# Performance work log

Hardware: AMD Instinct MI355X
Metric: run time of the kernel (lower is better)

## Reference

```python
import jax, jax.numpy as jnp
import numpy as np

N = 100000   # skill_num
D = 128      # skill_embed_dim
E = 500000   # edges per relation
S = 16384    # queried skills
NEG_SLOPE = 0.2


def _gat(x, edge_index, W, att_src, att_dst, bias):
    # PyG GATConv, heads=1, add_self_loops=True, eval mode (no dropout)
    n = x.shape[0]
    loops = jnp.arange(n)
    src = jnp.concatenate([edge_index[0], loops])
    dst = jnp.concatenate([edge_index[1], loops])
    h = x @ W                              # [N, D]
    a_src = h @ att_src                    # [N]
    a_dst = h @ att_dst                    # [N]
    e = jax.nn.leaky_relu(a_src[src] + a_dst[dst], NEG_SLOPE)  # [E+N]
    emax = jax.ops.segment_max(e, dst, num_segments=n)
    ex = jnp.exp(e - emax[dst])
    denom = jax.ops.segment_sum(ex, dst, num_segments=n)
    alpha = ex / (denom[dst] + 1e-16)
    out = jax.ops.segment_sum(alpha[:, None] * h[src], dst, num_segments=n)
    return out + bias


def _sage(x, edge_index, Wl, bl, Wr):
    # PyG SAGEConv, aggr='mean', root_weight=True (lin_r has no bias)
    n = x.shape[0]
    src, dst = edge_index[0], edge_index[1]
    ones = jnp.ones((src.shape[0],), dtype=x.dtype)
    deg = jax.ops.segment_sum(ones, dst, num_segments=n)
    agg = jax.ops.segment_sum(x[src], dst, num_segments=n)
    agg = agg / jnp.maximum(deg, 1.0)[:, None]
    return agg @ Wl + bl + x @ Wr


def setup_inputs() -> dict:
    key = jax.random.key(0)
    ks = jax.random.split(key, 16)
    sc = 1.0 / np.sqrt(D)
    inp = {
        "s": jax.random.randint(ks[0], (S,), 0, N),
        "t_s": 0,
        "t_e": 12,
        "ei_parent": jax.random.randint(ks[1], (2, E), 0, N),
        "ei_child": jax.random.randint(ks[2], (2, E), 0, N),
        "ei_relate": jax.random.randint(ks[3], (2, E), 0, N),
        "emb": jax.random.normal(ks[4], (N, D), dtype=jnp.float32),
        # GAT is_parent params
        "Wp": jax.random.normal(ks[5], (D, D), dtype=jnp.float32) * sc,
        "asp": jax.random.normal(ks[6], (D,), dtype=jnp.float32) * sc,
        "adp": jax.random.normal(ks[7], (D,), dtype=jnp.float32) * sc,
        "bp": jnp.zeros((D,), dtype=jnp.float32),
        # GAT is_child params
        "Wc": jax.random.normal(ks[8], (D, D), dtype=jnp.float32) * sc,
        "asc": jax.random.normal(ks[9], (D,), dtype=jnp.float32) * sc,
        "adc": jax.random.normal(ks[10], (D,), dtype=jnp.float32) * sc,
        "bc": jnp.zeros((D,), dtype=jnp.float32),
        # SAGE relate params
        "Wl": jax.random.normal(ks[11], (D, D), dtype=jnp.float32) * sc,
        "bl": jnp.zeros((D,), dtype=jnp.float32),
        "Wr": jax.random.normal(ks[12], (D, D), dtype=jnp.float32) * sc,
    }
    return inp


def reference(s, t_s, t_e, ei_parent, ei_child, ei_relate, emb,
              Wp, asp, adp, bp, Wc, asc, adc, bc, Wl, bl, Wr):
    out_parent = _gat(emb, ei_parent, Wp, asp, adp, bp)
    out_child = _gat(emb, ei_child, Wc, asc, adc, bc)
    out_relate = _sage(emb, ei_relate, Wl, bl, Wr)
    # HeteroConv(aggr='mean') over the three relation outputs
    node_out = (out_parent + out_child + out_relate) / 3.0
    return node_out[s, :]
```

## Files before the change

### kernel.cpp

```cpp
#include <hip/hip_runtime.h>

#define D 128
#define CAP 64
#define OVF_CAP 1024

typedef short bf16x8 __attribute__((ext_vector_type(8)));
typedef short short4v __attribute__((ext_vector_type(4)));
typedef float f32x4 __attribute__((ext_vector_type(4)));

__device__ __forceinline__ short f2bf(float f) {
  unsigned u = __builtin_bit_cast(unsigned, f);
  unsigned r = (u + 0x7fffu + ((u >> 16) & 1u)) >> 16;
  return (short)r;
}
__device__ __forceinline__ float bflo(unsigned r) {
  return __builtin_bit_cast(float, r << 16);
}
__device__ __forceinline__ float bfhi(unsigned r) {
  return __builtin_bit_cast(float, r & 0xffff0000u);
}


__global__ void k_setup(const float* __restrict__ Wp, const float* __restrict__ asp,
                        const float* __restrict__ adp, const float* __restrict__ Wc,
                        const float* __restrict__ asc, const float* __restrict__ adc,
                        const float* __restrict__ bp, const float* __restrict__ bc,
                        const float* __restrict__ bl, const float* __restrict__ Wl,
                        const float* __restrict__ Wr,
                        float* __restrict__ v, short* __restrict__ wpack,
                        int* __restrict__ qid, int* __restrict__ counters,
                        int* __restrict__ deg3, int N, int S3) {
  int i = blockIdx.x * blockDim.x + threadIdx.x;
  int stride = gridDim.x * blockDim.x;
  for (int k = i; k < N; k += stride) qid[k] = -1;
  for (int k = i; k < S3; k += stride) deg3[k] = 0;
  if (i < 16) counters[i] = 0;

  for (int idx = i; idx < 16 * 8 * 64 * 8; idx += stride) {
    int j    = idx & 7;
    int lane = (idx >> 3) & 63;
    int nt   = (idx >> 9) & 7;
    int kt   = idx >> 12;
    int o = kt >> 2;
    int c = (kt & 3) * 32 + (lane >> 4) * 8 + j;
    int n = nt * 16 + (lane & 15);
    const float* W = (o == 0) ? Wp : (o == 1) ? Wc : (o == 2) ? Wl : Wr;
    wpack[idx] = f2bf(W[c * D + n]);
  }

  if (blockIdx.x == 0 && threadIdx.x < 128) {
    int k = threadIdx.x;
    float s0 = 0.f, s1 = 0.f, s2 = 0.f, s3 = 0.f;
    for (int d = 0; d < D; ++d) {
      float wp = Wp[k * D + d], wc = Wc[k * D + d];
      s0 += wp * asp[d]; s1 += wp * adp[d];
      s2 += wc * asc[d]; s3 += wc * adc[d];
    }
    v[k] = s0; v[D + k] = s1; v[2 * D + k] = s2; v[3 * D + k] = s3;
    v[4 * D + k] = bp[k] + bc[k] + bl[k];
  }
}

__global__ void k_pre(const int* __restrict__ s, int* __restrict__ qid,
                      int* __restrict__ uniq, int* __restrict__ counters, int S,
                      const float* __restrict__ emb, const float* __restrict__ v,
                      float* __restrict__ a_sp, float* __restrict__ a_dp,
                      float* __restrict__ a_sc, float* __restrict__ a_dc,
                      unsigned* __restrict__ ebf, int N) {
  int gtid = blockIdx.x * blockDim.x + threadIdx.x;
  if (gtid < S) {
    int n = s[gtid];
    if (atomicCAS(&qid[n], -1, -2) == -1) {
      int u = atomicAdd(&counters[0], 1);
      uniq[u] = n;
      qid[n] = u;
    }
  }
  int node = gtid >> 6;
  int lane = threadIdx.x & 63;
  if (node >= N) return;
  float2 x2 = ((const float2*)(emb + (size_t)node * D))[lane];
  unsigned p = ((unsigned)(unsigned short)f2bf(x2.x)) |
               (((unsigned)(unsigned short)f2bf(x2.y)) << 16);
  ebf[(size_t)node * 64 + lane] = p;
  float2 v0 = ((const float2*)(v))[lane];
  float2 v1 = ((const float2*)(v + D))[lane];
  float2 v2 = ((const float2*)(v + 2 * D))[lane];
  float2 v3 = ((const float2*)(v + 3 * D))[lane];
  float s0 = x2.x * v0.x + x2.y * v0.y;
  float s1 = x2.x * v1.x + x2.y * v1.y;
  float s2 = x2.x * v2.x + x2.y * v2.y;
  float s3 = x2.x * v3.x + x2.y * v3.y;
  for (int o = 32; o > 0; o >>= 1) {
    s0 += __shfl_down(s0, o);
    s1 += __shfl_down(s1, o);
    s2 += __shfl_down(s2, o);
    s3 += __shfl_down(s3, o);
  }
  if (lane == 0) { a_sp[node] = s0; a_dp[node] = s1; a_sc[node] = s2; a_dc[node] = s3; }
}

__global__ void __launch_bounds__(256) k_filter(
    const int* __restrict__ eiP, const int* __restrict__ eiC, const int* __restrict__ eiR,
    const int* __restrict__ qid,
    int* __restrict__ bktP, int* __restrict__ bktC, int* __restrict__ bktR,
    int* __restrict__ degP, int* __restrict__ degC, int* __restrict__ degR,
    int2* __restrict__ ovf, int* __restrict__ counters, int E) {
  int rel = blockIdx.y;
  const int* ei = (rel == 0) ? eiP : (rel == 1) ? eiC : eiR;
  int* bkt      = (rel == 0) ? bktP : (rel == 1) ? bktC : bktR;
  int* deg      = (rel == 0) ? degP : (rel == 1) ? degC : degR;
  int e = blockIdx.x * 256 + threadIdx.x;
  if (e >= E) return;
  int dst = ei[E + e];
  int u = qid[dst];
  if (u < 0) return;
  int src = ei[e];
  int pos = atomicAdd(&deg[u], 1);
  if (pos < CAP) {
    bkt[u * CAP + pos] = src;
  } else {
    int o = atomicAdd(&counters[4 + rel], 1);
    if (o < OVF_CAP) { int2 t; t.x = src; t.y = u; ovf[rel * OVF_CAP + o] = t; }
  }
}

__global__ void __launch_bounds__(256) k_accum(
    const int* __restrict__ bktP, const int* __restrict__ bktC, const int* __restrict__ bktR,
    const int* __restrict__ degP, const int* __restrict__ degC, const int* __restrict__ degR,
    const float* __restrict__ a_sp, const float* __restrict__ a_dp,
    const float* __restrict__ a_sc, const float* __restrict__ a_dc,
    const unsigned* __restrict__ ebf, const int* __restrict__ uniq,
    const int* __restrict__ counters, const int2* __restrict__ ovf,
    float* __restrict__ num_p, float* __restrict__ num_c, float* __restrict__ sum_r,
    float* __restrict__ den_p, float* __restrict__ den_c) {
  int U = counters[0];
  int u = blockIdx.x * 4 + (threadIdx.x >> 6);
  if (u >= U) return;
  int lane = threadIdx.x & 63;
  int rel = blockIdx.y;
  const int* bkt = (rel == 0) ? bktP : (rel == 1) ? bktC : bktR;
  const int* deg = (rel == 0) ? degP : (rel == 1) ? degC : degR;
  float* num     = (rel == 0) ? num_p : (rel == 1) ? num_c : sum_r;

  int m = deg[u];
  int mc = (m < CAP) ? m : CAP;
  int L = counters[4 + rel];
  if (L > OVF_CAP) L = OVF_CAP;
  const int* b0 = bkt + u * CAP;
  float2 acc; acc.x = 0.f; acc.y = 0.f;

  int srcl = (lane < mc) ? b0[lane] : 0;
  float wl = 0.f;
  bool gat = (rel != 2);
  float denl = 0.f;
  if (gat) {
    const float* a_s = (rel == 0) ? a_sp : a_sc;
    const float* a_d = (rel == 0) ? a_dp : a_dc;
    int n = uniq[u];
    float adn = a_d[n];
    if (lane < mc) {
      float t = a_s[srcl] + adn;
      t = t >= 0.f ? t : 0.2f * t;
      wl = __expf(t);
    }
    denl = wl;
  } else {
    wl = (lane < mc) ? 1.f : 0.f;
  }

  int i = 0;
  for (; i + 4 <= mc; i += 4) {
    int s0 = __shfl(srcl, i),     s1 = __shfl(srcl, i + 1);
    int s2 = __shfl(srcl, i + 2), s3 = __shfl(srcl, i + 3);
    float w0 = __shfl(wl, i),     w1 = __shfl(wl, i + 1);
    float w2 = __shfl(wl, i + 2), w3 = __shfl(wl, i + 3);
    unsigned r0 = ebf[(size_t)s0 * 64 + lane];
    unsigned r1 = ebf[(size_t)s1 * 64 + lane];
    unsigned r2 = ebf[(size_t)s2 * 64 + lane];
    unsigned r3 = ebf[(size_t)s3 * 64 + lane];
    acc.x += w0 * bflo(r0) + w1 * bflo(r1) + w2 * bflo(r2) + w3 * bflo(r3);
    acc.y += w0 * bfhi(r0) + w1 * bfhi(r1) + w2 * bfhi(r2) + w3 * bfhi(r3);
  }
  for (; i < mc; ++i) {
    int si = __shfl(srcl, i);
    float wi = __shfl(wl, i);
    unsigned r = ebf[(size_t)si * 64 + lane];
    acc.x += wi * bflo(r);
    acc.y += wi * bfhi(r);
  }

  if (gat) {
    const float* a_s = (rel == 0) ? a_sp : a_sc;
    const float* a_d = (rel == 0) ? a_dp : a_dc;
    float adn = a_d[uniq[u]];
    float denx = 0.f;
    for (int l = 0; l < L; ++l) {
      int2 ov = ovf[rel * OVF_CAP + l];
      if (ov.y == u) {
        float t = a_s[ov.x] + adn;
        t = t >= 0.f ? t : 0.2f * t;
        float w = __expf(t);
        unsigned r = ebf[(size_t)ov.x * 64 + lane];
        acc.x += w * bflo(r); acc.y += w * bfhi(r);
        if (lane == 0) denx += w;
      }
    }
    for (int o = 32; o > 0; o >>= 1) denl += __shfl_down(denl, o);
    if (lane == 0) { ((rel == 0) ? den_p : den_c)[u] = denl + denx; }
  } else {
    for (int l = 0; l < L; ++l) {
      int2 ov = ovf[2 * OVF_CAP + l];
      if (ov.y == u) {
        unsigned r = ebf[(size_t)ov.x * 64 + lane];
        acc.x += bflo(r); acc.y += bfhi(r);
      }
    }
  }
  ((float2*)(num + (size_t)u * D))[lane] = acc;
}

__global__ void __launch_bounds__(256) k_final(
    const float* __restrict__ num_p, const float* __restrict__ num_c,
    const float* __restrict__ sum_r, const float* __restrict__ emb,
    const int* __restrict__ uniq, const int* __restrict__ counters,
    const float* __restrict__ a_sp, const float* __restrict__ a_dp,
    const float* __restrict__ a_sc, const float* __restrict__ a_dc,
    const float* __restrict__ den_p, const float* __restrict__ den_c,
    const int* __restrict__ deg_r, const float* __restrict__ vvec,
    const short* __restrict__ wpack, float* __restrict__ outU) {
  __shared__ short A_lds[16 * 64 * 8];
  int U = counters[0];
  int u0 = blockIdx.x * 16;
  if (u0 >= U) return;
  int tid = threadIdx.x;

  {
    int m = tid >> 4;
    int oc = tid & 15;
    int u = u0 + m;
    int uu = (u < U) ? u : u0;
    int n = uniq[uu];
    float tP = a_sp[n] + a_dp[n]; tP = tP >= 0.f ? tP : 0.2f * tP;
    float wP = __expf(tP);
    float rP = 1.f / (den_p[uu] + wP);
    float tC = a_sc[n] + a_dc[n]; tC = tC >= 0.f ? tC : 0.2f * tC;
    float wC = __expf(tC);
    float rC = 1.f / (den_c[uu] + wC);
    float dg = (float)deg_r[uu]; if (dg < 1.f) dg = 1.f;
    float rdeg = 1.f / dg;
#pragma unroll
    for (int half = 0; half < 2; ++half) {
      int c4 = oc * 8 + half * 4;
      int q = (c4 >> 3) & 3;
      int j0 = c4 & 7;
      int ktc = c4 >> 5;
      float4 e4  = *(const float4*)(emb   + (size_t)n  * D + c4);
      float4 np4 = *(const float4*)(num_p + (size_t)uu * D + c4);
      float4 nc4 = *(const float4*)(num_c + (size_t)uu * D + c4);
      float4 sr4 = *(const float4*)(sum_r + (size_t)uu * D + c4);
      float4 z[4];
      z[0].x = (np4.x + wP * e4.x) * rP; z[0].y = (np4.y + wP * e4.y) * rP;
      z[0].z = (np4.z + wP * e4.z) * rP; z[0].w = (np4.w + wP * e4.w) * rP;
      z[1].x = (nc4.x + wC * e4.x) * rC; z[1].y = (nc4.y + wC * e4.y) * rC;
      z[1].z = (nc4.z + wC * e4.z) * rC; z[1].w = (nc4.w + wC * e4.w) * rC;
      z[2].x = sr4.x * rdeg; z[2].y = sr4.y * rdeg;
      z[2].z = sr4.z * rdeg; z[2].w = sr4.w * rdeg;
      z[3] = e4;
#pragma unroll
      for (int o = 0; o < 4; ++o) {
        int kt = o * 4 + ktc;
        short4v s4;
        s4.x = f2bf(z[o].x); s4.y = f2bf(z[o].y);
        s4.z = f2bf(z[o].z); s4.w = f2bf(z[o].w);
        *(short4v*)&A_lds[(kt * 64 + q * 16 + m) * 8 + j0] = s4;
      }
    }
  }
  __syncthreads();

  int w = tid >> 6;
  int lane = tid & 63;
  f32x4 acc0 = {0.f, 0.f, 0.f, 0.f};
  f32x4 acc1 = {0.f, 0.f, 0.f, 0.f};
  const bf16x8* wp = (const bf16x8*)wpack;
#pragma unroll
  for (int kt = 0; kt < 16; ++kt) {
    bf16x8 a  = *(const bf16x8*)&A_lds[(kt * 64 + lane) * 8];
    bf16x8 b0 = wp[(kt * 8 + 2 * w) * 64 + lane];
    bf16x8 b1 = wp[(kt * 8 + 2 * w + 1) * 64 + lane];
    acc0 = __builtin_amdgcn_mfma_f32_16x16x32_bf16(a, b0, acc0, 0, 0, 0);
    acc1 = __builtin_amdgcn_mfma_f32_16x16x32_bf16(a, b1, acc1, 0, 0, 0);
  }

  int col0 = 2 * w * 16 + (lane & 15);
  int col1 = col0 + 16;
  int r0 = (lane >> 4) * 4;
  float b0v = vvec[4 * D + col0] * (1.f / 3.f);
  float b1v = vvec[4 * D + col1] * (1.f / 3.f);
#pragma unroll
  for (int reg = 0; reg < 4; ++reg) {
    int u = u0 + r0 + reg;
    if (u < U) {
      outU[(size_t)u * D + col0] = acc0[reg] * (1.f / 3.f) + b0v;
      outU[(size_t)u * D + col1] = acc1[reg] * (1.f / 3.f) + b1v;
    }
  }
}

__global__ void k_gather(const int* __restrict__ s, const int* __restrict__ qid,
                         const float* __restrict__ outU, float* __restrict__ out, int S) {
  int idx = blockIdx.x * blockDim.x + threadIdx.x;
  if (idx >= S * D) return;
  int i = idx >> 7;
  int d = idx & (D - 1);
  int u = qid[s[i]];
  out[idx] = outU[(size_t)u * D + d];
}


extern "C" void kernel_launch(void* const* d_in, const int* in_sizes, int n_in,
                              void* d_out, int out_size, void* d_ws, size_t ws_size,
                              hipStream_t stream) {
  const int*   s   = (const int*)d_in[0];
  const int*   eip = (const int*)d_in[3];
  const int*   eic = (const int*)d_in[4];
  const int*   eir = (const int*)d_in[5];
  const float* emb = (const float*)d_in[6];
  const float* Wp  = (const float*)d_in[7];
  const float* asp = (const float*)d_in[8];
  const float* adp = (const float*)d_in[9];
  const float* bp  = (const float*)d_in[10];
  const float* Wc  = (const float*)d_in[11];
  const float* asc = (const float*)d_in[12];
  const float* adc = (const float*)d_in[13];
  const float* bc  = (const float*)d_in[14];
  const float* Wl  = (const float*)d_in[15];
  const float* bl  = (const float*)d_in[16];
  const float* Wr  = (const float*)d_in[17];
  float* out = (float*)d_out;

  const int S = in_sizes[0];
  const int E = in_sizes[3] / 2;
  const int N = in_sizes[6] / D;

  char* base = (char*)d_ws;
  size_t off = 0;
  auto carve = [&](size_t bytes) -> char* {
    char* q = base + off;
    off += (bytes + 255) & ~(size_t)255;
    return q;
  };
  float*    a_sp     = (float*)carve((size_t)N * 4);
  float*    a_dp     = (float*)carve((size_t)N * 4);
  float*    a_sc     = (float*)carve((size_t)N * 4);
  float*    a_dc     = (float*)carve((size_t)N * 4);
  int*      qid      = (int*)carve((size_t)N * 4);
  unsigned* ebf      = (unsigned*)carve((size_t)N * 64 * 4);
  int*      uniq     = (int*)carve((size_t)S * 4);
  int*      counters = (int*)carve(64);
  float*    vvec     = (float*)carve(5 * D * 4);
  short*    wpack    = (short*)carve((size_t)16 * 8 * 64 * 8 * 2);
  float*    num_p    = (float*)carve((size_t)S * D * 4);
  float*    den_p    = (float*)carve((size_t)S * 4);
  float*    num_c    = (float*)carve((size_t)S * D * 4);
  float*    den_c    = (float*)carve((size_t)S * 4);
  float*    sum_r    = (float*)carve((size_t)S * D * 4);
  float*    outU     = (float*)carve((size_t)S * D * 4);
  int*      degP     = (int*)carve((size_t)S * 4);
  int*      degC     = (int*)carve((size_t)S * 4);
  int*      degR     = (int*)carve((size_t)S * 4);
  int*      bktP     = (int*)carve((size_t)S * CAP * 4);
  int*      bktC     = (int*)carve((size_t)S * CAP * 4);
  int*      bktR     = (int*)carve((size_t)S * CAP * 4);
  int2*     ovf      = (int2*)carve((size_t)3 * OVF_CAP * 8);
  (void)ws_size; (void)n_in; (void)out_size;

  k_setup<<<256, 256, 0, stream>>>(Wp, asp, adp, Wc, asc, adc, bp, bc, bl, Wl, Wr,
                                   vvec, wpack, qid, counters, degP, N, 3 * S);

  k_pre<<<(N * 64 + 255) / 256, 256, 0, stream>>>(s, qid, uniq, counters, S,
                                                  emb, vvec, a_sp, a_dp, a_sc, a_dc,
                                                  ebf, N);

  k_filter<<<dim3((E + 255) / 256, 3), 256, 0, stream>>>(
      eip, eic, eir, qid, bktP, bktC, bktR, degP, degC, degR, ovf, counters, E);

  k_accum<<<dim3((S + 3) / 4, 3), 256, 0, stream>>>(
      bktP, bktC, bktR, degP, degC, degR,
      a_sp, a_dp, a_sc, a_dc, ebf, uniq, counters, ovf,
      num_p, num_c, sum_r, den_p, den_c);

  k_final<<<(S + 15) / 16, 256, 0, stream>>>(num_p, num_c, sum_r, emb, uniq, counters,
                                             a_sp, a_dp, a_sc, a_dc, den_p, den_c, degR,
                                             vvec, wpack, outU);
  k_gather<<<(S * D + 255) / 256, 256, 0, stream>>>(s, qid, outU, out, S);
}
```

Baseline: 213.2 us.

## Fuse neighbor accumulation into final MFMA kernel and widen k_pre per-lane loads

Measured after the change: 199.6 us. -6.4%, faster.

```diff
diff --git a/kernel.cpp b/kernel.cpp
--- a/kernel.cpp
+++ b/kernel.cpp
@@ -5,19 +5,21 @@
 #define OVF_CAP 1024
 
 typedef short bf16x8 __attribute__((ext_vector_type(8)));
-typedef short short4v __attribute__((ext_vector_type(4)));
 typedef float f32x4 __attribute__((ext_vector_type(4)));
 
-__device__ __forceinline__ short f2bf(float f) {
+__device__ __forceinline__ unsigned short f2bf(float f) {
   unsigned u = __builtin_bit_cast(unsigned, f);
   unsigned r = (u + 0x7fffu + ((u >> 16) & 1u)) >> 16;
-  return (short)r;
+  return (unsigned short)r;
 }
 __device__ __forceinline__ float bflo(unsigned r) {
   return __builtin_bit_cast(float, r << 16);
 }
 __device__ __forceinline__ float bfhi(unsigned r) {
   return __builtin_bit_cast(float, r & 0xffff0000u);
+}
+__device__ __forceinline__ float lrelu(float t) {
+  return t >= 0.f ? t : 0.2f * t;
 }
 
 
@@ -27,7 +29,7 @@
                         const float* __restrict__ bp, const float* __restrict__ bc,
                         const float* __restrict__ bl, const float* __restrict__ Wl,
                         const float* __restrict__ Wr,
-                        float* __restrict__ v, short* __restrict__ wpack,
+                        float* __restrict__ v, unsigned short* __restrict__ wpack,
                         int* __restrict__ qid, int* __restrict__ counters,
                         int* __restrict__ deg3, int N, int S3) {
   int i = blockIdx.x * blockDim.x + threadIdx.x;
@@ -76,28 +78,31 @@
       qid[n] = u;
     }
   }
-  int node = gtid >> 6;
   int lane = threadIdx.x & 63;
+  int node = (gtid >> 6) * 2 + (lane >> 5);
+  int c = lane & 31;
   if (node >= N) return;
-  float2 x2 = ((const float2*)(emb + (size_t)node * D))[lane];
-  unsigned p = ((unsigned)(unsigned short)f2bf(x2.x)) |
-               (((unsigned)(unsigned short)f2bf(x2.y)) << 16);
-  ebf[(size_t)node * 64 + lane] = p;
-  float2 v0 = ((const float2*)(v))[lane];
-  float2 v1 = ((const float2*)(v + D))[lane];
-  float2 v2 = ((const float2*)(v + 2 * D))[lane];
-  float2 v3 = ((const float2*)(v + 3 * D))[lane];
-  float s0 = x2.x * v0.x + x2.y * v0.y;
-  float s1 = x2.x * v1.x + x2.y * v1.y;
-  float s2 = x2.x * v2.x + x2.y * v2.y;
-  float s3 = x2.x * v3.x + x2.y * v3.y;
-  for (int o = 32; o > 0; o >>= 1) {
+  float4 x4 = ((const float4*)(emb + (size_t)node * D))[c];
+  uint2 p;
+  p.x = ((unsigned)f2bf(x4.x)) | (((unsigned)f2bf(x4.y)) << 16);
+  p.y = ((unsigned)f2bf(x4.z)) | (((unsigned)f2bf(x4.w)) << 16);
+  ((uint2*)ebf)[(size_t)node * 32 + c] = p;
+  float4 v0 = ((const float4*)(v))[c];
+  float4 v1 = ((const float4*)(v + D))[c];
+  float4 v2 = ((const float4*)(v + 2 * D))[c];
+  float4 v3 = ((const float4*)(v + 3 * D))[c];
+  float s0 = x4.x * v0.x + x4.y * v0.y + x4.z * v0.z + x4.w * v0.w;
+  float s1 = x4.x * v1.x + x4.y * v1.y + x4.z * v1.z + x4.w * v1.w;
+  float s2 = x4.x * v2.x + x4.y * v2.y + x4.z * v2.z + x4.w * v2.w;
+  float s3 = x4.x * v3.x + x4.y * v3.y + x4.z * v3.z + x4.w * v3.w;
+#pragma unroll
+  for (int o = 16; o > 0; o >>= 1) {
     s0 += __shfl_down(s0, o);
     s1 += __shfl_down(s1, o);
     s2 += __shfl_down(s2, o);
     s3 += __shfl_down(s3, o);
   }
-  if (lane == 0) { a_sp[node] = s0; a_dp[node] = s1; a_sc[node] = s2; a_dc[node] = s3; }
+  if (c == 0) { a_sp[node] = s0; a_dp[node] = s1; a_sc[node] = s2; a_dc[node] = s3; }
 }
 
 __global__ void __launch_bounds__(256) k_filter(
@@ -125,162 +130,125 @@
   }
 }
 
-__global__ void __launch_bounds__(256) k_accum(
+__global__ void __launch_bounds__(256) k_fused(
     const int* __restrict__ bktP, const int* __restrict__ bktC, const int* __restrict__ bktR,
     const int* __restrict__ degP, const int* __restrict__ degC, const int* __restrict__ degR,
     const float* __restrict__ a_sp, const float* __restrict__ a_dp,
     const float* __restrict__ a_sc, const float* __restrict__ a_dc,
-    const unsigned* __restrict__ ebf, const int* __restrict__ uniq,
-    const int* __restrict__ counters, const int2* __restrict__ ovf,
-    float* __restrict__ num_p, float* __restrict__ num_c, float* __restrict__ sum_r,
-    float* __restrict__ den_p, float* __restrict__ den_c) {
-  int U = counters[0];
-  int u = blockIdx.x * 4 + (threadIdx.x >> 6);
-  if (u >= U) return;
-  int lane = threadIdx.x & 63;
-  int rel = blockIdx.y;
-  const int* bkt = (rel == 0) ? bktP : (rel == 1) ? bktC : bktR;
-  const int* deg = (rel == 0) ? degP : (rel == 1) ? degC : degR;
-  float* num     = (rel == 0) ? num_p : (rel == 1) ? num_c : sum_r;
-
-  int m = deg[u];
-  int mc = (m < CAP) ? m : CAP;
-  int L = counters[4 + rel];
-  if (L > OVF_CAP) L = OVF_CAP;
-  const int* b0 = bkt + u * CAP;
-  float2 acc; acc.x = 0.f; acc.y = 0.f;
-
-  int srcl = (lane < mc) ? b0[lane] : 0;
-  float wl = 0.f;
-  bool gat = (rel != 2);
-  float denl = 0.f;
-  if (gat) {
-    const float* a_s = (rel == 0) ? a_sp : a_sc;
-    const float* a_d = (rel == 0) ? a_dp : a_dc;
-    int n = uniq[u];
-    float adn = a_d[n];
-    if (lane < mc) {
-      float t = a_s[srcl] + adn;
-      t = t >= 0.f ? t : 0.2f * t;
-      wl = __expf(t);
-    }
-    denl = wl;
-  } else {
-    wl = (lane < mc) ? 1.f : 0.f;
-  }
-
-  int i = 0;
-  for (; i + 4 <= mc; i += 4) {
-    int s0 = __shfl(srcl, i),     s1 = __shfl(srcl, i + 1);
-    int s2 = __shfl(srcl, i + 2), s3 = __shfl(srcl, i + 3);
-    float w0 = __shfl(wl, i),     w1 = __shfl(wl, i + 1);
-    float w2 = __shfl(wl, i + 2), w3 = __shfl(wl, i + 3);
-    unsigned r0 = ebf[(size_t)s0 * 64 + lane];
-    unsigned r1 = ebf[(size_t)s1 * 64 + lane];
-    unsigned r2 = ebf[(size_t)s2 * 64 + lane];
-    unsigned r3 = ebf[(size_t)s3 * 64 + lane];
-    acc.x += w0 * bflo(r0) + w1 * bflo(r1) + w2 * bflo(r2) + w3 * bflo(r3);
-    acc.y += w0 * bfhi(r0) + w1 * bfhi(r1) + w2 * bfhi(r2) + w3 * bfhi(r3);
-  }
-  for (; i < mc; ++i) {
-    int si = __shfl(srcl, i);
-    float wi = __shfl(wl, i);
-    unsigned r = ebf[(size_t)si * 64 + lane];
-    acc.x += wi * bflo(r);
-    acc.y += wi * bfhi(r);
-  }
-
-  if (gat) {
-    const float* a_s = (rel == 0) ? a_sp : a_sc;
-    const float* a_d = (rel == 0) ? a_dp : a_dc;
-    float adn = a_d[uniq[u]];
-    float denx = 0.f;
-    for (int l = 0; l < L; ++l) {
-      int2 ov = ovf[rel * OVF_CAP + l];
-      if (ov.y == u) {
-        float t = a_s[ov.x] + adn;
-        t = t >= 0.f ? t : 0.2f * t;
-        float w = __expf(t);
-        unsigned r = ebf[(size_t)ov.x * 64 + lane];
-        acc.x += w * bflo(r); acc.y += w * bfhi(r);
-        if (lane == 0) denx += w;
-      }
-    }
-    for (int o = 32; o > 0; o >>= 1) denl += __shfl_down(denl, o);
-    if (lane == 0) { ((rel == 0) ? den_p : den_c)[u] = denl + denx; }
-  } else {
-    for (int l = 0; l < L; ++l) {
-      int2 ov = ovf[2 * OVF_CAP + l];
-      if (ov.y == u) {
-        unsigned r = ebf[(size_t)ov.x * 64 + lane];
-        acc.x += bflo(r); acc.y += bfhi(r);
-      }
-    }
-  }
-  ((float2*)(num + (size_t)u * D))[lane] = acc;
-}
-
-__global__ void __launch_bounds__(256) k_final(
-    const float* __restrict__ num_p, const float* __restrict__ num_c,
-    const float* __restrict__ sum_r, const float* __restrict__ emb,
+    const unsigned* __restrict__ ebf, const float* __restrict__ emb,
     const int* __restrict__ uniq, const int* __restrict__ counters,
-    const float* __restrict__ a_sp, const float* __restrict__ a_dp,
-    const float* __restrict__ a_sc, const float* __restrict__ a_dc,
-    const float* __restrict__ den_p, const float* __restrict__ den_c,
-    const int* __restrict__ deg_r, const float* __restrict__ vvec,
-    const short* __restrict__ wpack, float* __restrict__ outU) {
-  __shared__ short A_lds[16 * 64 * 8];
+    const int2* __restrict__ ovf, const float* __restrict__ vvec,
+    const unsigned short* __restrict__ wpack, float* __restrict__ outU) {
+  __shared__ unsigned short A_lds[16 * 64 * 8];
   int U = counters[0];
   int u0 = blockIdx.x * 16;
   if (u0 >= U) return;
   int tid = threadIdx.x;
-
-  {
-    int m = tid >> 4;
-    int oc = tid & 15;
-    int u = u0 + m;
-    int uu = (u < U) ? u : u0;
-    int n = uniq[uu];
-    float tP = a_sp[n] + a_dp[n]; tP = tP >= 0.f ? tP : 0.2f * tP;
-    float wP = __expf(tP);
-    float rP = 1.f / (den_p[uu] + wP);
-    float tC = a_sc[n] + a_dc[n]; tC = tC >= 0.f ? tC : 0.2f * tC;
-    float wC = __expf(tC);
-    float rC = 1.f / (den_c[uu] + wC);
-    float dg = (float)deg_r[uu]; if (dg < 1.f) dg = 1.f;
-    float rdeg = 1.f / dg;
-#pragma unroll
-    for (int half = 0; half < 2; ++half) {
-      int c4 = oc * 8 + half * 4;
-      int q = (c4 >> 3) & 3;
-      int j0 = c4 & 7;
-      int ktc = c4 >> 5;
-      float4 e4  = *(const float4*)(emb   + (size_t)n  * D + c4);
-      float4 np4 = *(const float4*)(num_p + (size_t)uu * D + c4);
-      float4 nc4 = *(const float4*)(num_c + (size_t)uu * D + c4);
-      float4 sr4 = *(const float4*)(sum_r + (size_t)uu * D + c4);
-      float4 z[4];
-      z[0].x = (np4.x + wP * e4.x) * rP; z[0].y = (np4.y + wP * e4.y) * rP;
-      z[0].z = (np4.z + wP * e4.z) * rP; z[0].w = (np4.w + wP * e4.w) * rP;
-      z[1].x = (nc4.x + wC * e4.x) * rC; z[1].y = (nc4.y + wC * e4.y) * rC;
-      z[1].z = (nc4.z + wC * e4.z) * rC; z[1].w = (nc4.w + wC * e4.w) * rC;
-      z[2].x = sr4.x * rdeg; z[2].y = sr4.y * rdeg;
-      z[2].z = sr4.z * rdeg; z[2].w = sr4.w * rdeg;
-      z[3] = e4;
-#pragma unroll
-      for (int o = 0; o < 4; ++o) {
-        int kt = o * 4 + ktc;
-        short4v s4;
-        s4.x = f2bf(z[o].x); s4.y = f2bf(z[o].y);
-        s4.z = f2bf(z[o].z); s4.w = f2bf(z[o].w);
-        *(short4v*)&A_lds[(kt * 64 + q * 16 + m) * 8 + j0] = s4;
-      }
-    }
-  }
-  __syncthreads();
-
   int w = tid >> 6;
   int lane = tid & 63;
+
+  const int* bkts[3] = {bktP, bktC, bktR};
+  const int* degs[3] = {degP, degC, degR};
+  int Lc[3];
+#pragma unroll
+  for (int r = 0; r < 3; ++r) {
+    int L = counters[4 + r];
+    Lc[r] = (L > OVF_CAP) ? OVF_CAP : L;
+  }
+
+  for (int t = 0; t < 4; ++t) {
+    int m = 4 * w + t;
+    int u = u0 + m;
+    float2 z[4];
+    if (u < U) {
+      int n = uniq[u];
+      float2 x2 = ((const float2*)(emb + (size_t)n * D))[lane];
+      float2 acc[3];
+      float den[2];
+#pragma unroll
+      for (int r = 0; r < 3; ++r) {
+        int dg = degs[r][u];
+        int mc = (dg < CAP) ? dg : CAP;
+        const int* b0 = bkts[r] + u * CAP;
+        int srcl = (lane < mc) ? b0[lane] : 0;
+        float wl = 0.f;
+        float adn = 0.f;
+        const float* a_s = (r == 0) ? a_sp : a_sc;
+        if (r < 2) {
+          adn = ((r == 0) ? a_dp : a_dc)[n];
+          if (lane < mc) wl = __expf(lrelu(a_s[srcl] + adn));
+        } else {
+          wl = (lane < mc) ? 1.f : 0.f;
+        }
+        float2 a; a.x = 0.f; a.y = 0.f;
+        int i = 0;
+        for (; i + 4 <= mc; i += 4) {
+          int s0 = __shfl(srcl, i),     s1 = __shfl(srcl, i + 1);
+          int s2 = __shfl(srcl, i + 2), s3 = __shfl(srcl, i + 3);
+          float w0 = __shfl(wl, i),     w1 = __shfl(wl, i + 1);
+          float w2 = __shfl(wl, i + 2), w3 = __shfl(wl, i + 3);
+          unsigned r0 = ebf[(size_t)s0 * 64 + lane];
+          unsigned r1 = ebf[(size_t)s1 * 64 + lane];
+          unsigned r2 = ebf[(size_t)s2 * 64 + lane];
+          unsigned r3 = ebf[(size_t)s3 * 64 + lane];
+          a.x += w0 * bflo(r0) + w1 * bflo(r1) + w2 * bflo(r2) + w3 * bflo(r3);
+          a.y += w0 * bfhi(r0) + w1 * bfhi(r1) + w2 * bfhi(r2) + w3 * bfhi(r3);
+        }
+        for (; i < mc; ++i) {
+          int si = __shfl(srcl, i);
+          float wi = __shfl(wl, i);
+          unsigned rr = ebf[(size_t)si * 64 + lane];
+          a.x += wi * bflo(rr);
+          a.y += wi * bfhi(rr);
+        }
+        float denx = 0.f;
+        if (dg > CAP) {
+          for (int l = 0; l < Lc[r]; ++l) {
+            int2 ov = ovf[r * OVF_CAP + l];
+            if (ov.y == u) {
+              float wv = 1.f;
+              if (r < 2) wv = __expf(lrelu(a_s[ov.x] + adn));
+              unsigned rr = ebf[(size_t)ov.x * 64 + lane];
+              a.x += wv * bflo(rr);
+              a.y += wv * bfhi(rr);
+              denx += wv;
+            }
+          }
+        }
+        if (r < 2) {
+          float dsum = wl;
+#pragma unroll
+          for (int o = 32; o > 0; o >>= 1) dsum += __shfl_down(dsum, o);
+          den[r] = __shfl(dsum, 0) + denx;
+        } else {
+          float dgc = (float)dg; if (dgc < 1.f) dgc = 1.f;
+          a.x *= (1.f / dgc); a.y *= (1.f / dgc);
+        }
+        acc[r] = a;
+      }
+      float wP = __expf(lrelu(a_sp[n] + a_dp[n]));
+      float rP = 1.f / (den[0] + wP);
+      float wC = __expf(lrelu(a_sc[n] + a_dc[n]));
+      float rC = 1.f / (den[1] + wC);
+      z[0].x = (acc[0].x + wP * x2.x) * rP; z[0].y = (acc[0].y + wP * x2.y) * rP;
+      z[1].x = (acc[1].x + wC * x2.x) * rC; z[1].y = (acc[1].y + wC * x2.y) * rC;
+      z[2] = acc[2];
+      z[3] = x2;
+    } else {
+      z[0].x = 0.f; z[0].y = 0.f; z[1] = z[0]; z[2] = z[0]; z[3] = z[0];
+    }
+    int ktc = lane >> 4;
+    int q = (lane >> 2) & 3;
+    int j0 = 2 * (lane & 3);
+#pragma unroll
+    for (int o = 0; o < 4; ++o) {
+      int kt = o * 4 + ktc;
+      unsigned pk = ((unsigned)f2bf(z[o].x)) | (((unsigned)f2bf(z[o].y)) << 16);
+      *(unsigned*)&A_lds[(kt * 64 + q * 16 + m) * 8 + j0] = pk;
+    }
+  }
+  __syncthreads();
+
   f32x4 acc0 = {0.f, 0.f, 0.f, 0.f};
   f32x4 acc1 = {0.f, 0.f, 0.f, 0.f};
   const bf16x8* wp = (const bf16x8*)wpack;
@@ -360,12 +328,7 @@
   int*      uniq     = (int*)carve((size_t)S * 4);
   int*      counters = (int*)carve(64);
   float*    vvec     = (float*)carve(5 * D * 4);
-  short*    wpack    = (short*)carve((size_t)16 * 8 * 64 * 8 * 2);
-  float*    num_p    = (float*)carve((size_t)S * D * 4);
-  float*    den_p    = (float*)carve((size_t)S * 4);
-  float*    num_c    = (float*)carve((size_t)S * D * 4);
-  float*    den_c    = (float*)carve((size_t)S * 4);
-  float*    sum_r    = (float*)carve((size_t)S * D * 4);
+  unsigned short* wpack = (unsigned short*)carve((size_t)16 * 8 * 64 * 8 * 2);
   float*    outU     = (float*)carve((size_t)S * D * 4);
   int*      degP     = (int*)carve((size_t)S * 4);
   int*      degC     = (int*)carve((size_t)S * 4);
@@ -379,20 +342,17 @@
   k_setup<<<256, 256, 0, stream>>>(Wp, asp, adp, Wc, asc, adc, bp, bc, bl, Wl, Wr,
                                    vvec, wpack, qid, counters, degP, N, 3 * S);
 
-  k_pre<<<(N * 64 + 255) / 256, 256, 0, stream>>>(s, qid, uniq, counters, S,
+  k_pre<<<(N * 32 + 255) / 256, 256, 0, stream>>>(s, qid, uniq, counters, S,
                                                   emb, vvec, a_sp, a_dp, a_sc, a_dc,
                                                   ebf, N);
 
   k_filter<<<dim3((E + 255) / 256, 3), 256, 0, stream>>>(
       eip, eic, eir, qid, bktP, bktC, bktR, degP, degC, degR, ovf, counters, E);
 
-  k_accum<<<dim3((S + 3) / 4, 3), 256, 0, stream>>>(
+  k_fused<<<(S + 15) / 16, 256, 0, stream>>>(
       bktP, bktC, bktR, degP, degC, degR,
-      a_sp, a_dp, a_sc, a_dc, ebf, uniq, counters, ovf,
-      num_p, num_c, sum_r, den_p, den_c);
-
-  k_final<<<(S + 15) / 16, 256, 0, stream>>>(num_p, num_c, sum_r, emb, uniq, counters,
-                                             a_sp, a_dp, a_sc, a_dc, den_p, den_c, degR,
-                                             vvec, wpack, outU);
+      a_sp, a_dp, a_sc, a_dc, ebf, emb, uniq, counters, ovf,
+      vvec, wpack, outU);
+
   k_gather<<<(S * D + 255) / 256, 256, 0, stream>>>(s, qid, outU, out, S);
 }
```
